# Performance work log

Hardware: AMD Instinct MI355X
Metric: run time of the kernel (lower is better)

The kernel has to match this reference:

```python
import jax, jax.numpy as jnp
import numpy as np

_SCAN_CHUNK = 32


def _causal_decay_scan(x, decay, init):
    """Inclusive scan out[t] = decay*out[t-1] + x[t], chunked closed form.
    x: [B,H,T,D], decay: [1,H,1], init: [B,H,D]. Returns [B,H,T,D]."""
    B, H, T, D = x.shape
    C = min(_SCAN_CHUNK, T)
    assert T % C == 0
    nC = T // C
    log_decay = jnp.log(jnp.clip(decay.astype(jnp.float32), 1e-8, None))  # [1,H,1]
    c_idx = jnp.arange(C, dtype=jnp.float32)
    log_p = log_decay[..., None] * c_idx.reshape(1, 1, C, 1)              # [1,H,C,1]
    p = jnp.exp(log_p)
    inv_p = jnp.exp(-log_p)
    init_p = jnp.exp(log_decay[..., None] * (c_idx + 1.0).reshape(1, 1, C, 1))
    # [nC, B, H, C, D] so lax.scan chains chunk states causally
    xc = x.reshape(B, H, nC, C, D).transpose(2, 0, 1, 3, 4).astype(jnp.float32)

    def step(state, chunk):  # state [B,H,D], chunk [B,H,C,D]
        cs = jnp.cumsum(chunk * inv_p, axis=2)
        out = cs * p + state[:, :, None, :] * init_p
        return out[:, :, -1, :], out

    _, outs = jax.lax.scan(step, init.astype(jnp.float32), xc)
    return outs.transpose(1, 2, 0, 3, 4).reshape(B, H, T, D).astype(x.dtype)


def _phi(x):
    return jax.nn.elu(x) + 1.0


def setup_inputs() -> dict:
    key = jax.random.key(0)
    ks = jax.random.split(key, 5)
    B, T, hidden, H = 4, 4096, 1024, 16
    s = 1.0 / np.sqrt(hidden)
    x = jax.random.normal(ks[0], (B, T, hidden), dtype=jnp.float32)
    Wqkv = jax.random.normal(ks[1], (3 * hidden, hidden), dtype=jnp.float32) * s
    Wout = jax.random.normal(ks[2], (hidden, hidden), dtype=jnp.float32) * s
    Wgate = jax.random.normal(ks[3], (hidden, hidden), dtype=jnp.float32) * s
    bgate = jnp.zeros((hidden,), dtype=jnp.float32)
    logit = float(np.log(0.95 / 0.05))  # sigmoid(logit) == 0.95
    decay_param = jnp.full((H,), logit, dtype=jnp.float32)
    return {"x": x, "Wqkv": Wqkv, "Wout": Wout, "Wgate": Wgate,
            "bgate": bgate, "decay_param": decay_param}


def reference(x, Wqkv, Wout, Wgate, bgate, decay_param):
    B, T, hidden = x.shape
    H = decay_param.shape[0]
    D = hidden // H
    qkv = x @ Wqkv.T                       # [B,T,3*hidden]
    q, k, v = jnp.split(qkv, 3, axis=-1)
    # [B,T,hidden] -> [B,H,T,D]
    q = q.reshape(B, T, H, D).transpose(0, 2, 1, 3)
    k = k.reshape(B, T, H, D).transpose(0, 2, 1, 3)
    v = v.reshape(B, T, H, D).transpose(0, 2, 1, 3)
    q = _phi(q)
    k = _phi(k)
    decay = jax.nn.sigmoid(decay_param).reshape(1, H, 1)
    kv_init = jnp.zeros((B, H, D), dtype=x.dtype)
    ksum_init = jnp.zeros((B, H, D), dtype=x.dtype)
    running_kv = _causal_decay_scan(k * v, decay, kv_init)
    running_ksum = _causal_decay_scan(k, decay, ksum_init)
    den = jnp.clip(jnp.sum(q * running_ksum, axis=-1, keepdims=True), 1e-6, None)
    out = q * running_kv / den             # [B,H,T,D]
    v_direct = v.transpose(0, 2, 1, 3).reshape(B, T, hidden)
    out = out.transpose(0, 2, 1, 3).reshape(B, T, hidden)
    g = jax.nn.sigmoid(out @ Wgate.T + bgate)
    out = g * out + (1.0 - g) * v_direct
    return out @ Wout.T
```

## Files before the change

### kernel.cpp

```cpp
#include <hip/hip_runtime.h>

typedef unsigned short u16;
typedef __bf16 bf16x8 __attribute__((ext_vector_type(8)));
typedef float f32x4 __attribute__((ext_vector_type(4)));

#define BB 4
#define TT 4096
#define HID 1024
#define NH 16
#define HD 64
#define BT (BB*TT)
#define NCH 128
#define LOG_NCH 7
#define CLEN (TT/NCH)

__device__ __forceinline__ float bf2f(u16 u) {
    return __uint_as_float(((unsigned)u) << 16);
}
__device__ __forceinline__ u16 f2bf(float f) {
    unsigned u = __float_as_uint(f);
    unsigned r = 0x7FFFu + ((u >> 16) & 1u);
    return (u16)((u + r) >> 16);
}
__device__ __forceinline__ float phi(float x) {
    return x > 0.f ? x + 1.f : __expf(x);
}
__device__ __forceinline__ float sigmoidf(float x) {
    return 1.f / (1.f + __expf(-x));
}

__global__ void f32_to_bf16_v4(const float4* __restrict__ in, u16* __restrict__ out, int n4) {
    int i = blockIdx.x * 256 + threadIdx.x;
    if (i >= n4) return;
    float4 f = in[i];
    ushort4 u;
    u.x = f2bf(f.x); u.y = f2bf(f.y); u.z = f2bf(f.z); u.w = f2bf(f.w);
    ((ushort4*)out)[i] = u;
}

template<int EPI>
__global__ __launch_bounds__(256)
void gemm_bt(const u16* __restrict__ A, const u16* __restrict__ Bm,
             int M, int N, int K, void* __restrict__ Cout,
             const float* __restrict__ bg,
             const u16* __restrict__ attn,
             const u16* __restrict__ qkv)
{
    __shared__ u16 As[128 * 64];
    __shared__ u16 Bs[128 * 64];
    const int tid  = threadIdx.x;
    const int wave = tid >> 6;
    const int lane = tid & 63;
    const int m0 = blockIdx.y * 128;
    const int n0 = blockIdx.x * 128;
    const int mw = (wave & 1) * 64;
    const int nw = (wave >> 1) * 64;
    const int r16 = lane & 15;

    f32x4 acc[4][4];
    #pragma unroll
    for (int i = 0; i < 4; ++i)
        #pragma unroll
        for (int j = 0; j < 4; ++j)
            acc[i][j] = (f32x4){0.f, 0.f, 0.f, 0.f};

    for (int k0 = 0; k0 < K; k0 += 64) {
        #pragma unroll
        for (int i = 0; i < 4; ++i) {
            int s   = i * 4 + wave;
            int idx = s * 64 + lane;
            int pr  = idx >> 3;
            int pc  = idx & 7;
            int lc  = pc ^ (pr & 7);
            const u16* gA = A  + (size_t)(m0 + pr) * K + k0 + lc * 8;
            const u16* gB = Bm + (size_t)(n0 + pr) * K + k0 + lc * 8;
            __builtin_amdgcn_global_load_lds(
                (const __attribute__((address_space(1))) void*)gA,
                (__attribute__((address_space(3))) void*)&As[s * 512], 16, 0, 0);
            __builtin_amdgcn_global_load_lds(
                (const __attribute__((address_space(1))) void*)gB,
                (__attribute__((address_space(3))) void*)&Bs[s * 512], 16, 0, 0);
        }
        __syncthreads();
        #pragma unroll
        for (int s2 = 0; s2 < 2; ++s2) {
            const int lcq = s2 * 4 + (lane >> 4);
            const int pcq = lcq ^ (r16 & 7);
            bf16x8 af[4], bq[4];
            #pragma unroll
            for (int i = 0; i < 4; ++i)
                af[i] = *(const bf16x8*)&As[(mw + i * 16 + r16) * 64 + pcq * 8];
            #pragma unroll
            for (int j = 0; j < 4; ++j)
                bq[j] = *(const bf16x8*)&Bs[(nw + j * 16 + r16) * 64 + pcq * 8];
            #pragma unroll
            for (int i = 0; i < 4; ++i)
                #pragma unroll
                for (int j = 0; j < 4; ++j)
                    acc[i][j] = __builtin_amdgcn_mfma_f32_16x16x32_bf16(af[i], bq[j], acc[i][j], 0, 0, 0);
        }
        __syncthreads();
    }

    #pragma unroll
    for (int i = 0; i < 4; ++i) {
        int rowb = m0 + mw + i * 16 + (lane >> 4) * 4;
        #pragma unroll
        for (int j = 0; j < 4; ++j) {
            int col = n0 + nw + j * 16 + r16;
            #pragma unroll
            for (int r = 0; r < 4; ++r) {
                float v = acc[i][j][r];
                size_t row = (size_t)(rowb + r);
                if (EPI == 0) {
                    ((u16*)Cout)[row * N + col] = f2bf(v);
                } else if (EPI == 1) {
                    float g  = sigmoidf(v + bg[col]);
                    float at = bf2f(attn[row * HID + col]);
                    float vd = bf2f(qkv[row * (3 * HID) + 2 * HID + col]);
                    ((u16*)Cout)[row * HID + col] = f2bf(g * at + (1.f - g) * vd);
                } else {
                    ((float*)Cout)[row * N + col] = v;
                }
            }
        }
    }
}

__global__ void scan_finals(const u16* __restrict__ qkv, const float* __restrict__ decay_param,
                            float* __restrict__ ckv, float* __restrict__ cks) {
    int g    = blockIdx.x * 4 + (threadIdx.x >> 6);
    int lane = threadIdx.x & 63;
    int c = g & (NCH - 1);
    int h = (g >> LOG_NCH) & (NH - 1);
    int b = g >> (LOG_NCH + 4);
    float decay = sigmoidf(decay_param[h]);
    const u16* kp = qkv + (size_t)(b * TT + c * CLEN) * (3 * HID) + HID + h * HD + lane;
    float skv = 0.f, sks = 0.f;
    for (int t = 0; t < CLEN; ++t) {
        float k = phi(bf2f(kp[0]));
        float v = bf2f(kp[HID]);
        skv = decay * skv + k * v;
        sks = decay * sks + k;
        kp += 3 * HID;
    }
    ckv[(size_t)g * 64 + lane] = skv;
    cks[(size_t)g * 64 + lane] = sks;
}

__global__ void scan_prefix(float* __restrict__ ckv, float* __restrict__ cks,
                            const float* __restrict__ decay_param) {
    int bh = blockIdx.x;
    int h  = bh & (NH - 1);
    int lane = threadIdx.x;
    float decay = sigmoidf(decay_param[h]);
    float dC = powf(decay, (float)CLEN);
    float* pkv = ckv + (size_t)bh * NCH * 64 + lane;
    float* pks = cks + (size_t)bh * NCH * 64 + lane;
    float fkv = 0.f, fks = 0.f;
    for (int c = 0; c < NCH; ++c) {
        float lkv = pkv[c * 64], lks = pks[c * 64];
        pkv[c * 64] = fkv; pks[c * 64] = fks;
        fkv = fkv * dC + lkv;
        fks = fks * dC + lks;
    }
}

__global__ void scan_apply(const u16* __restrict__ qkv, const float* __restrict__ decay_param,
                           const float* __restrict__ ckv, const float* __restrict__ cks,
                           u16* __restrict__ attn) {
    int g    = blockIdx.x * 4 + (threadIdx.x >> 6);
    int lane = threadIdx.x & 63;
    int c = g & (NCH - 1);
    int h = (g >> LOG_NCH) & (NH - 1);
    int b = g >> (LOG_NCH + 4);
    float decay = sigmoidf(decay_param[h]);
    float skv = ckv[(size_t)g * 64 + lane];
    float sks = cks[(size_t)g * 64 + lane];
    const u16* qp = qkv + (size_t)(b * TT + c * CLEN) * (3 * HID) + h * HD + lane;
    u16* op = attn + (size_t)(b * TT + c * CLEN) * HID + h * HD + lane;
    for (int t = 0; t < CLEN; ++t) {
        float q = phi(bf2f(qp[0]));
        float k = phi(bf2f(qp[HID]));
        float v = bf2f(qp[2 * HID]);
        skv = decay * skv + k * v;
        sks = decay * sks + k;
        float s = q * sks;
        s += __shfl_xor(s, 32);
        s += __shfl_xor(s, 16);
        s += __shfl_xor(s, 8);
        s += __shfl_xor(s, 4);
        s += __shfl_xor(s, 2);
        s += __shfl_xor(s, 1);
        float den = fmaxf(s, 1e-6f);
        op[0] = f2bf(q * skv / den);
        qp += 3 * HID;
        op += HID;
    }
}

extern "C" void kernel_launch(void* const* d_in, const int* in_sizes, int n_in,
                              void* d_out, int out_size, void* d_ws, size_t ws_size,
                              hipStream_t stream) {
    const float* x     = (const float*)d_in[0];
    const float* Wqkv  = (const float*)d_in[1];
    const float* Wout  = (const float*)d_in[2];
    const float* Wgate = (const float*)d_in[3];
    const float* bgate = (const float*)d_in[4];
    const float* decay = (const float*)d_in[5];

    u16* xb     = (u16*)d_ws;
    u16* wqkvb  = xb    + (size_t)BT * HID;
    u16* wgateb = wqkvb + (size_t)3 * HID * HID;
    u16* woutb  = wgateb + (size_t)HID * HID;
    u16* qkvb   = woutb + (size_t)HID * HID;
    u16* out2b  = qkvb  + (size_t)BT * 3 * HID;
    float* ckv  = (float*)(out2b + (size_t)BT * HID);
    float* cks  = ckv + (size_t)BB * NH * NCH * HD;
    u16* attnb  = xb;

    {
        int n4 = BT * HID / 4;
        f32_to_bf16_v4<<<n4 / 256, 256, 0, stream>>>((const float4*)x, xb, n4);
        n4 = 3 * HID * HID / 4;
        f32_to_bf16_v4<<<n4 / 256, 256, 0, stream>>>((const float4*)Wqkv, wqkvb, n4);
        n4 = HID * HID / 4;
        f32_to_bf16_v4<<<n4 / 256, 256, 0, stream>>>((const float4*)Wgate, wgateb, n4);
        f32_to_bf16_v4<<<n4 / 256, 256, 0, stream>>>((const float4*)Wout, woutb, n4);
    }

    gemm_bt<0><<<dim3(3 * HID / 128, BT / 128), 256, 0, stream>>>(
        xb, wqkvb, BT, 3 * HID, HID, qkvb, nullptr, nullptr, nullptr);

    scan_finals<<<BB * NH * NCH / 4, 256, 0, stream>>>(qkvb, decay, ckv, cks);
    scan_prefix<<<BB * NH, 64, 0, stream>>>(ckv, cks, decay);
    scan_apply<<<BB * NH * NCH / 4, 256, 0, stream>>>(qkvb, decay, ckv, cks, attnb);

    gemm_bt<1><<<dim3(HID / 128, BT / 128), 256, 0, stream>>>(
        attnb, wgateb, BT, HID, HID, out2b, bgate, attnb, qkvb);

    gemm_bt<2><<<dim3(HID / 128, BT / 128), 256, 0, stream>>>(
        out2b, woutb, BT, HID, HID, d_out, nullptr, nullptr, nullptr);
}
```

Before: 413.8 us.

## Fuse conversions, vectorize scan kernels, use 64-row tiles for square GEMMs

Merges the four f32-to-bf16 conversion launches into one kernel. The scan_finals and scan_apply kernels now process four head dimensions per thread with ushort4/float4 loads and 16-lane reductions, and use a reciprocal in place of per-element division. The gate and output GEMMs move to a new 64x128-tile variant so the 1024-wide outputs launch twice as many blocks and fill more CUs. The tradeoff is less data reuse per block in those GEMMs and fewer threads in the scans.

```diff
diff --git a/kernel.cpp b/kernel.cpp
--- a/kernel.cpp
+++ b/kernel.cpp
@@ -28,14 +28,28 @@
 __device__ __forceinline__ float sigmoidf(float x) {
     return 1.f / (1.f + __expf(-x));
 }
-
-__global__ void f32_to_bf16_v4(const float4* __restrict__ in, u16* __restrict__ out, int n4) {
+__device__ __forceinline__ float4 u4_to_f4(ushort4 u) {
+    return make_float4(bf2f(u.x), bf2f(u.y), bf2f(u.z), bf2f(u.w));
+}
+
+#define CN1 (BT*HID/4)
+#define CN2 (3*HID*HID/4)
+#define CN3 (HID*HID/4)
+#define CN4 (HID*HID/4)
+__global__ void convert_all(const float4* __restrict__ x,    const float4* __restrict__ wqkv,
+                            const float4* __restrict__ wgate, const float4* __restrict__ wout,
+                            ushort4* __restrict__ xb,    ushort4* __restrict__ wqkvb,
+                            ushort4* __restrict__ wgateb, ushort4* __restrict__ woutb) {
     int i = blockIdx.x * 256 + threadIdx.x;
-    if (i >= n4) return;
-    float4 f = in[i];
+    const float4* src; ushort4* dst; int j;
+    if (i < CN1)                 { src = x;     dst = xb;     j = i; }
+    else if (i < CN1+CN2)        { src = wqkv;  dst = wqkvb;  j = i - CN1; }
+    else if (i < CN1+CN2+CN3)    { src = wgate; dst = wgateb; j = i - CN1 - CN2; }
+    else                         { src = wout;  dst = woutb;  j = i - CN1 - CN2 - CN3; }
+    float4 f = src[j];
     ushort4 u;
     u.x = f2bf(f.x); u.y = f2bf(f.y); u.z = f2bf(f.z); u.w = f2bf(f.w);
-    ((ushort4*)out)[i] = u;
+    dst[j] = u;
 }
 
 template<int EPI>
@@ -127,25 +141,118 @@
     }
 }
 
+template<int EPI>
+__global__ __launch_bounds__(256)
+void gemm_bt_sm(const u16* __restrict__ A, const u16* __restrict__ Bm,
+                int M, int N, int K, void* __restrict__ Cout,
+                const float* __restrict__ bg,
+                const u16* __restrict__ attn,
+                const u16* __restrict__ qkv)
+{
+    __shared__ u16 As[64 * 64];
+    __shared__ u16 Bs[128 * 64];
+    const int tid  = threadIdx.x;
+    const int wave = tid >> 6;
+    const int lane = tid & 63;
+    const int m0 = blockIdx.y * 64;
+    const int n0 = blockIdx.x * 128;
+    const int mw = (wave & 1) * 32;
+    const int nw = (wave >> 1) * 64;
+    const int r16 = lane & 15;
+
+    f32x4 acc[2][4];
+    #pragma unroll
+    for (int i = 0; i < 2; ++i)
+        #pragma unroll
+        for (int j = 0; j < 4; ++j)
+            acc[i][j] = (f32x4){0.f, 0.f, 0.f, 0.f};
+
+    for (int k0 = 0; k0 < K; k0 += 64) {
+        #pragma unroll
+        for (int i = 0; i < 4; ++i) {
+            int s   = i * 4 + wave;
+            int idx = s * 64 + lane;
+            int pr  = idx >> 3;
+            int pc  = idx & 7;
+            int lc  = pc ^ (pr & 7);
+            const u16* gB = Bm + (size_t)(n0 + pr) * K + k0 + lc * 8;
+            __builtin_amdgcn_global_load_lds(
+                (const __attribute__((address_space(1))) void*)gB,
+                (__attribute__((address_space(3))) void*)&Bs[s * 512], 16, 0, 0);
+            if (i < 2) {
+                const u16* gA = A + (size_t)(m0 + pr) * K + k0 + lc * 8;
+                __builtin_amdgcn_global_load_lds(
+                    (const __attribute__((address_space(1))) void*)gA,
+                    (__attribute__((address_space(3))) void*)&As[s * 512], 16, 0, 0);
+            }
+        }
+        __syncthreads();
+        #pragma unroll
+        for (int s2 = 0; s2 < 2; ++s2) {
+            const int lcq = s2 * 4 + (lane >> 4);
+            const int pcq = lcq ^ (r16 & 7);
+            bf16x8 af[2], bq[4];
+            #pragma unroll
+            for (int i = 0; i < 2; ++i)
+                af[i] = *(const bf16x8*)&As[(mw + i * 16 + r16) * 64 + pcq * 8];
+            #pragma unroll
+            for (int j = 0; j < 4; ++j)
+                bq[j] = *(const bf16x8*)&Bs[(nw + j * 16 + r16) * 64 + pcq * 8];
+            #pragma unroll
+            for (int i = 0; i < 2; ++i)
+                #pragma unroll
+                for (int j = 0; j < 4; ++j)
+                    acc[i][j] = __builtin_amdgcn_mfma_f32_16x16x32_bf16(af[i], bq[j], acc[i][j], 0, 0, 0);
+        }
+        __syncthreads();
+    }
+
+    #pragma unroll
+    for (int i = 0; i < 2; ++i) {
+        int rowb = m0 + mw + i * 16 + (lane >> 4) * 4;
+        #pragma unroll
+        for (int j = 0; j < 4; ++j) {
+            int col = n0 + nw + j * 16 + r16;
+            #pragma unroll
+            for (int r = 0; r < 4; ++r) {
+                float v = acc[i][j][r];
+                size_t row = (size_t)(rowb + r);
+                if (EPI == 1) {
+                    float g  = sigmoidf(v + bg[col]);
+                    float at = bf2f(attn[row * HID + col]);
+                    float vd = bf2f(qkv[row * (3 * HID) + 2 * HID + col]);
+                    ((u16*)Cout)[row * HID + col] = f2bf(g * at + (1.f - g) * vd);
+                } else {
+                    ((float*)Cout)[row * N + col] = v;
+                }
+            }
+        }
+    }
+}
+
 __global__ void scan_finals(const u16* __restrict__ qkv, const float* __restrict__ decay_param,
                             float* __restrict__ ckv, float* __restrict__ cks) {
-    int g    = blockIdx.x * 4 + (threadIdx.x >> 6);
-    int lane = threadIdx.x & 63;
+    int g  = blockIdx.x * 16 + (threadIdx.x >> 4);
+    int sl = threadIdx.x & 15;
     int c = g & (NCH - 1);
     int h = (g >> LOG_NCH) & (NH - 1);
     int b = g >> (LOG_NCH + 4);
     float decay = sigmoidf(decay_param[h]);
-    const u16* kp = qkv + (size_t)(b * TT + c * CLEN) * (3 * HID) + HID + h * HD + lane;
-    float skv = 0.f, sks = 0.f;
+    const u16* kp = qkv + (size_t)(b * TT + c * CLEN) * (3 * HID) + HID + h * HD + sl * 4;
+    float4 skv = make_float4(0.f, 0.f, 0.f, 0.f);
+    float4 sks = make_float4(0.f, 0.f, 0.f, 0.f);
     for (int t = 0; t < CLEN; ++t) {
-        float k = phi(bf2f(kp[0]));
-        float v = bf2f(kp[HID]);
-        skv = decay * skv + k * v;
-        sks = decay * sks + k;
+        float4 k = u4_to_f4(*(const ushort4*)kp);
+        float4 v = u4_to_f4(*(const ushort4*)(kp + HID));
+        k.x = phi(k.x); k.y = phi(k.y); k.z = phi(k.z); k.w = phi(k.w);
+        skv.x = decay * skv.x + k.x * v.x;  skv.y = decay * skv.y + k.y * v.y;
+        skv.z = decay * skv.z + k.z * v.z;  skv.w = decay * skv.w + k.w * v.w;
+        sks.x = decay * sks.x + k.x;        sks.y = decay * sks.y + k.y;
+        sks.z = decay * sks.z + k.z;        sks.w = decay * sks.w + k.w;
         kp += 3 * HID;
     }
-    ckv[(size_t)g * 64 + lane] = skv;
-    cks[(size_t)g * 64 + lane] = sks;
+    *(float4*)(ckv + (size_t)g * 64 + sl * 4) = skv;
+    *(float4*)(cks + (size_t)g * 64 + sl * 4) = sks;
 }
 
 __global__ void scan_prefix(float* __restrict__ ckv, float* __restrict__ cks,
@@ -169,31 +276,36 @@
 __global__ void scan_apply(const u16* __restrict__ qkv, const float* __restrict__ decay_param,
                            const float* __restrict__ ckv, const float* __restrict__ cks,
                            u16* __restrict__ attn) {
-    int g    = blockIdx.x * 4 + (threadIdx.x >> 6);
-    int lane = threadIdx.x & 63;
+    int g  = blockIdx.x * 16 + (threadIdx.x >> 4);
+    int sl = threadIdx.x & 15;
     int c = g & (NCH - 1);
     int h = (g >> LOG_NCH) & (NH - 1);
     int b = g >> (LOG_NCH + 4);
     float decay = sigmoidf(decay_param[h]);
-    float skv = ckv[(size_t)g * 64 + lane];
-    float sks = cks[(size_t)g * 64 + lane];
-    const u16* qp = qkv + (size_t)(b * TT + c * CLEN) * (3 * HID) + h * HD + lane;
-    u16* op = attn + (size_t)(b * TT + c * CLEN) * HID + h * HD + lane;
+    float4 skv = *(const float4*)(ckv + (size_t)g * 64 + sl * 4);
+    float4 sks = *(const float4*)(cks + (size_t)g * 64 + sl * 4);
+    const u16* qp = qkv + (size_t)(b * TT + c * CLEN) * (3 * HID) + h * HD + sl * 4;
+    u16* op = attn + (size_t)(b * TT + c * CLEN) * HID + h * HD + sl * 4;
     for (int t = 0; t < CLEN; ++t) {
-        float q = phi(bf2f(qp[0]));
-        float k = phi(bf2f(qp[HID]));
-        float v = bf2f(qp[2 * HID]);
-        skv = decay * skv + k * v;
-        sks = decay * sks + k;
-        float s = q * sks;
-        s += __shfl_xor(s, 32);
-        s += __shfl_xor(s, 16);
+        float4 q = u4_to_f4(*(const ushort4*)qp);
+        float4 k = u4_to_f4(*(const ushort4*)(qp + HID));
+        float4 v = u4_to_f4(*(const ushort4*)(qp + 2 * HID));
+        q.x = phi(q.x); q.y = phi(q.y); q.z = phi(q.z); q.w = phi(q.w);
+        k.x = phi(k.x); k.y = phi(k.y); k.z = phi(k.z); k.w = phi(k.w);
+        skv.x = decay * skv.x + k.x * v.x;  skv.y = decay * skv.y + k.y * v.y;
+        skv.z = decay * skv.z + k.z * v.z;  skv.w = decay * skv.w + k.w * v.w;
+        sks.x = decay * sks.x + k.x;        sks.y = decay * sks.y + k.y;
+        sks.z = decay * sks.z + k.z;        sks.w = decay * sks.w + k.w;
+        float s = q.x * sks.x + q.y * sks.y + q.z * sks.z + q.w * sks.w;
         s += __shfl_xor(s, 8);
         s += __shfl_xor(s, 4);
         s += __shfl_xor(s, 2);
         s += __shfl_xor(s, 1);
-        float den = fmaxf(s, 1e-6f);
-        op[0] = f2bf(q * skv / den);
+        float inv = 1.f / fmaxf(s, 1e-6f);
+        ushort4 o;
+        o.x = f2bf(q.x * skv.x * inv); o.y = f2bf(q.y * skv.y * inv);
+        o.z = f2bf(q.z * skv.z * inv); o.w = f2bf(q.w * skv.w * inv);
+        *(ushort4*)op = o;
         qp += 3 * HID;
         op += HID;
     }
@@ -219,26 +331,20 @@
     float* cks  = ckv + (size_t)BB * NH * NCH * HD;
     u16* attnb  = xb;
 
-    {
-        int n4 = BT * HID / 4;
-        f32_to_bf16_v4<<<n4 / 256, 256, 0, stream>>>((const float4*)x, xb, n4);
-        n4 = 3 * HID * HID / 4;
-        f32_to_bf16_v4<<<n4 / 256, 256, 0, stream>>>((const float4*)Wqkv, wqkvb, n4);
-        n4 = HID * HID / 4;
-        f32_to_bf16_v4<<<n4 / 256, 256, 0, stream>>>((const float4*)Wgate, wgateb, n4);
-        f32_to_bf16_v4<<<n4 / 256, 256, 0, stream>>>((const float4*)Wout, woutb, n4);
-    }
+    convert_all<<<(CN1 + CN2 + CN3 + CN4) / 256, 256, 0, stream>>>(
+        (const float4*)x, (const float4*)Wqkv, (const float4*)Wgate, (const float4*)Wout,
+        (ushort4*)xb, (ushort4*)wqkvb, (ushort4*)wgateb, (ushort4*)woutb);
 
     gemm_bt<0><<<dim3(3 * HID / 128, BT / 128), 256, 0, stream>>>(
         xb, wqkvb, BT, 3 * HID, HID, qkvb, nullptr, nullptr, nullptr);
 
-    scan_finals<<<BB * NH * NCH / 4, 256, 0, stream>>>(qkvb, decay, ckv, cks);
+    scan_finals<<<BB * NH * NCH / 16, 256, 0, stream>>>(qkvb, decay, ckv, cks);
     scan_prefix<<<BB * NH, 64, 0, stream>>>(ckv, cks, decay);
-    scan_apply<<<BB * NH * NCH / 4, 256, 0, stream>>>(qkvb, decay, ckv, cks, attnb);
-
-    gemm_bt<1><<<dim3(HID / 128, BT / 128), 256, 0, stream>>>(
+    scan_apply<<<BB * NH * NCH / 16, 256, 0, stream>>>(qkvb, decay, ckv, cks, attnb);
+
+    gemm_bt_sm<1><<<dim3(HID / 128, BT / 64), 256, 0, stream>>>(
         attnb, wgateb, BT, HID, HID, out2b, bgate, attnb, qkvb);
 
-    gemm_bt<2><<<dim3(HID / 128, BT / 128), 256, 0, stream>>>(
+    gemm_bt_sm<2><<<dim3(HID / 128, BT / 64), 256, 0, stream>>>(
         out2b, woutb, BT, HID, HID, d_out, nullptr, nullptr, nullptr);
 }
```

Result: faster. 398.5 us (-3.7%).
